# Performance work log

Measured on AMD Instinct MI355X. Metric: run time of the kernel, lower is better.

## Reference

```python
import jax, jax.numpy as jnp
import numpy as np

N_HOPS = 3
N_NODES = 500000  # n_users + n_items


def setup_inputs() -> dict:
    key = jax.random.key(0)
    k1, k2, k3, k4, k5 = jax.random.split(key, 5)
    n_users, n_items, d, nnz = 100000, 400000, 64, 1250000
    return {
        "user_embed": jax.random.normal(k1, (n_users, d), dtype=jnp.float32),
        "item_embed": jax.random.normal(k2, (n_items, d), dtype=jnp.float32),
        "adj_row": jax.random.randint(k3, (nnz,), 0, n_users + n_items, dtype=jnp.int32),
        "adj_col": jax.random.randint(k4, (nnz,), 0, n_users + n_items, dtype=jnp.int32),
        "adj_val": jax.random.uniform(k5, (nnz,), dtype=jnp.float32),
        "n_users": n_users,
    }


def reference(user_embed, item_embed, adj_row, adj_col, adj_val, n_users):
    # all_embed: [N, d]
    all_embed = jnp.concatenate([user_embed, item_embed], axis=0)

    def spmm(x):
        # sparse @ dense: gather source-node features, scale by edge value,
        # scatter-add into destination rows. COO SpMM == SpecialSpmm.
        msgs = adj_val[:, None] * x[adj_col]          # [nnz, d]
        return jax.ops.segment_sum(msgs, adj_row, num_segments=N_NODES)

    agg = all_embed
    embs = [all_embed]
    for _ in range(N_HOPS):
        agg = spmm(agg)
        embs.append(agg)
    embs = jnp.stack(embs, axis=1)  # [N, n_hops+1, d]
    return embs[:n_users], embs[n_users:]
```

## Files before the change

### kernel.cpp

```cpp
#include <hip/hip_runtime.h>


#define DFEAT 64
#define ELLW 8

typedef float f32x4 __attribute__((ext_vector_type(4)));

__global__ void gc_zero(int4* __restrict__ p, int n4) {
    int i = blockIdx.x * blockDim.x + threadIdx.x;
    if (i < n4) p[i] = make_int4(0, 0, 0, 0);
}

__global__ void gc_fat(const float4* __restrict__ user4,
                       const float4* __restrict__ item4,
                       float4* __restrict__ out4,
                       const int* __restrict__ row, const int* __restrict__ col,
                       const float* __restrict__ val,
                       int* __restrict__ cnt, float2* __restrict__ ell,
                       int* __restrict__ ovfcnt, int4* __restrict__ ovf,
                       int n_users, int n_nodes, int nnz, int initB) {
    int b = blockIdx.x;
    if (b < initB) {
        int tid = b * blockDim.x + threadIdx.x;
        if (tid >= n_nodes * 16) return;
        int node = tid >> 4;
        int q = tid & 15;
        float4 v = (node < n_users) ? user4[(size_t)node * 16 + q]
                                    : item4[(size_t)(node - n_users) * 16 + q];
        out4[(size_t)node * 64 + q] = v;
    } else {
        int i = (b - initB) * blockDim.x + threadIdx.x;
        if (i >= nnz) return;
        int r = row[i];
        int pos = atomicAdd(&cnt[r], 1);
        int cq = col[i] << 6;
        if (pos < ELLW) {
            ell[(size_t)r * ELLW + pos] = make_float2(__int_as_float(cq), val[i]);
        } else {
            int o = atomicAdd(ovfcnt, 1);
            ovf[o] = make_int4(r, cq, __float_as_int(val[i]), 0);
        }
    }
}

__global__ void gc_hop(const int* __restrict__ cnt,
                       const float4* __restrict__ ell4,
                       float* __restrict__ out, int hop, int n_nodes) {
    int tid = blockIdx.x * blockDim.x + threadIdx.x;
    int l = tid & 7;
    int r = tid >> 3;
    if (r >= n_nodes) return;
    int c = cnt[r];
    if (c > ELLW) c = ELLW;
    const float4* src4 = (const float4*)out;
    int lane_off = (hop - 1) * 16 + l * 2;
    float4 a0 = make_float4(0.f, 0.f, 0.f, 0.f);
    float4 a1 = make_float4(0.f, 0.f, 0.f, 0.f);
    int e = 0;
    for (; e + 2 <= c; e += 2) {
        float4 s = ell4[(size_t)r * (ELLW / 2) + (e >> 1)];
        int i0 = __float_as_int(s.x) + lane_off;
        int i1 = __float_as_int(s.z) + lane_off;
        float4 x0a = src4[i0], x0b = src4[i0 + 1];
        float4 x1a = src4[i1], x1b = src4[i1 + 1];
        float v0 = s.y, v1 = s.w;
        a0.x += v0 * x0a.x; a0.y += v0 * x0a.y; a0.z += v0 * x0a.z; a0.w += v0 * x0a.w;
        a1.x += v0 * x0b.x; a1.y += v0 * x0b.y; a1.z += v0 * x0b.z; a1.w += v0 * x0b.w;
        a0.x += v1 * x1a.x; a0.y += v1 * x1a.y; a0.z += v1 * x1a.z; a0.w += v1 * x1a.w;
        a1.x += v1 * x1b.x; a1.y += v1 * x1b.y; a1.z += v1 * x1b.z; a1.w += v1 * x1b.w;
    }
    if (e < c) {
        float2 s = ((const float2*)ell4)[(size_t)r * ELLW + e];
        int i0 = __float_as_int(s.x) + lane_off;
        float4 x0a = src4[i0], x0b = src4[i0 + 1];
        float v0 = s.y;
        a0.x += v0 * x0a.x; a0.y += v0 * x0a.y; a0.z += v0 * x0a.z; a0.w += v0 * x0a.w;
        a1.x += v0 * x0b.x; a1.y += v0 * x0b.y; a1.z += v0 * x0b.z; a1.w += v0 * x0b.w;
    }
    size_t dq = (size_t)r * 64 + (size_t)hop * 16 + l * 2;
    float4* o4 = (float4*)out;
    if (hop == 3) {
        f32x4 n0 = {a0.x, a0.y, a0.z, a0.w};
        f32x4 n1 = {a1.x, a1.y, a1.z, a1.w};
        __builtin_nontemporal_store(n0, (f32x4*)o4 + dq);
        __builtin_nontemporal_store(n1, (f32x4*)o4 + dq + 1);
    } else {
        o4[dq] = a0;
        o4[dq + 1] = a1;
    }
}

__global__ void gc_ovf(const int* __restrict__ ovfcnt, const int4* __restrict__ ovf,
                       float* __restrict__ out, int hop) {
    int gtid = blockIdx.x * blockDim.x + threadIdx.x;
    int wave = gtid >> 6;
    int lane = gtid & 63;
    int nw = (gridDim.x * blockDim.x) >> 6;
    int cntv = *ovfcnt;
    size_t src_base = (size_t)(hop - 1) * 64 + lane;
    size_t dst_base = (size_t)hop * 64 + lane;
    for (int e = wave; e < cntv; e += nw) {
        int4 ed = ovf[e];
        int r = ed.x;
        int cq = ed.y;
        float v = __int_as_float(ed.z);
        float x = out[(size_t)cq * 4 + src_base];
        unsafeAtomicAdd(&out[(size_t)r * 256 + dst_base], v * x);
    }
}

__global__ void gc_init_out_full(const float4* __restrict__ user4,
                                 const float4* __restrict__ item4,
                                 float4* __restrict__ out4,
                                 int n_users, int n_nodes) {
    int tid = blockIdx.x * blockDim.x + threadIdx.x;
    if (tid >= n_nodes * 16) return;
    int node = tid >> 4;
    int q = tid & 15;
    float4 v = (node < n_users) ? user4[(size_t)node * 16 + q]
                                : item4[(size_t)(node - n_users) * 16 + q];
    float4 z = make_float4(0.f, 0.f, 0.f, 0.f);
    float4* p = out4 + (size_t)node * 64 + q;
    p[0] = v; p[16] = z; p[32] = z; p[48] = z;
}

__global__ void gc_spmm_atomic(const int* __restrict__ adj_row,
                               const int* __restrict__ adj_col,
                               const float* __restrict__ adj_val,
                               float* __restrict__ out, int hop, int nnz) {
    long long tid = (long long)blockIdx.x * blockDim.x + threadIdx.x;
    int e = (int)(tid >> 6);
    int j = (int)(tid & 63);
    if (e >= nnz) return;
    int r = adj_row[e];
    int c = adj_col[e];
    float v = adj_val[e];
    float x = out[(size_t)c * 256 + (size_t)(hop - 1) * 64 + j];
    unsafeAtomicAdd(&out[(size_t)r * 256 + (size_t)hop * 64 + j], v * x);
}

extern "C" void kernel_launch(void* const* d_in, const int* in_sizes, int n_in,
                              void* d_out, int out_size, void* d_ws, size_t ws_size,
                              hipStream_t stream) {
    const float* user_embed = (const float*)d_in[0];
    const float* item_embed = (const float*)d_in[1];
    const int*   adj_row    = (const int*)d_in[2];
    const int*   adj_col    = (const int*)d_in[3];
    const float* adj_val    = (const float*)d_in[4];
    const int n_users = in_sizes[0] / DFEAT;
    const int n_items = in_sizes[1] / DFEAT;
    const int n_nodes = n_users + n_items;
    const int nnz     = in_sizes[2];
    float* out = (float*)d_out;
    float4* out4 = (float4*)out;

    const int threads = 256;

    size_t off = 0;
    auto carve = [&](size_t bytes) { size_t o = off; off = (off + bytes + 255) & ~(size_t)255; return o; };
    size_t o_cnt    = carve((size_t)n_nodes * 4);
    size_t o_ovfcnt = carve(256);
    size_t zero_end = off;
    size_t o_ell    = carve((size_t)n_nodes * ELLW * 8);
    size_t o_ovf    = carve((size_t)nnz * 16);
    size_t needed = off;

    if (ws_size < needed) {
        int init_blocks = (n_nodes * 16 + threads - 1) / threads;
        hipLaunchKernelGGL(gc_init_out_full, dim3(init_blocks), dim3(threads), 0, stream,
                           (const float4*)user_embed, (const float4*)item_embed,
                           out4, n_users, n_nodes);
        long long spmm_total = (long long)nnz * 64;
        int spmm_blocks = (int)((spmm_total + threads - 1) / threads);
        for (int h = 1; h <= 3; ++h) {
            hipLaunchKernelGGL(gc_spmm_atomic, dim3(spmm_blocks), dim3(threads), 0, stream,
                               adj_row, adj_col, adj_val, out, h, nnz);
        }
        return;
    }

    char* ws = (char*)d_ws;
    int*    cnt    = (int*)(ws + o_cnt);
    int*    ovfcnt = (int*)(ws + o_ovfcnt);
    float2* ell    = (float2*)(ws + o_ell);
    int4*   ovf    = (int4*)(ws + o_ovf);

    int zn4 = (int)((zero_end - o_cnt) / 16);
    int zero_blocks = (zn4 + threads - 1) / threads;
    hipLaunchKernelGGL(gc_zero, dim3(zero_blocks), dim3(threads), 0, stream,
                       (int4*)(ws + o_cnt), zn4);

    int initB = (n_nodes * 16 + threads - 1) / threads;
    int scatB = (nnz + threads - 1) / threads;
    hipLaunchKernelGGL(gc_fat, dim3(initB + scatB), dim3(threads), 0, stream,
                       (const float4*)user_embed, (const float4*)item_embed, out4,
                       adj_row, adj_col, adj_val, cnt, ell, ovfcnt, ovf,
                       n_users, n_nodes, nnz, initB);

    long long hop_threads = (long long)n_nodes * 8;
    int hop_blocks = (int)((hop_threads + threads - 1) / threads);
    const int ovf_blocks = 256;
    for (int h = 1; h <= 3; ++h) {
        hipLaunchKernelGGL(gc_hop, dim3(hop_blocks), dim3(threads), 0, stream,
                           cnt, (const float4*)ell, out, h, n_nodes);
        hipLaunchKernelGGL(gc_ovf, dim3(ovf_blocks), dim3(threads), 0, stream,
                           ovfcnt, ovf, out, h);
    }
}
```

Before: 390.1 us.

## Gather neighbor features from bf16 shadow copies and widen ELL width

Keeps a bf16 shadow of each hop's embeddings (written alongside the fp32 output) and gathers neighbor rows from it in the SpMM hop, halving gathered bytes. ELL width grows from 8 to 12 so fewer edges fall into the atomic overflow path, and a fixup kernel refreshes shadow rows touched by overflow atomics. The fp32 output stores become nontemporal. This adds bf16 rounding error that compounds across hops, plus extra shadow writes and a small extra kernel per hop.

```diff
diff --git a/kernel.cpp b/kernel.cpp
--- a/kernel.cpp
+++ b/kernel.cpp
@@ -2,9 +2,20 @@
 
 
 #define DFEAT 64
-#define ELLW 8
+#define ELLW 12
 
 typedef float f32x4 __attribute__((ext_vector_type(4)));
+
+__device__ inline unsigned bf16rne(float x) {
+    unsigned u = __float_as_uint(x);
+    u += 0x7FFF + ((u >> 16) & 1);
+    return u;
+}
+__device__ inline unsigned pack2(float lo, float hi) {
+    return (bf16rne(lo) >> 16) | (bf16rne(hi) & 0xFFFF0000u);
+}
+__device__ inline float bflo(unsigned w) { return __uint_as_float(w << 16); }
+__device__ inline float bfhi(unsigned w) { return __uint_as_float(w & 0xFFFF0000u); }
 
 __global__ void gc_zero(int4* __restrict__ p, int n4) {
     int i = blockIdx.x * blockDim.x + threadIdx.x;
@@ -13,7 +24,7 @@
 
 __global__ void gc_fat(const float4* __restrict__ user4,
                        const float4* __restrict__ item4,
-                       float4* __restrict__ out4,
+                       float4* __restrict__ out4, uint2* __restrict__ shadow0,
                        const int* __restrict__ row, const int* __restrict__ col,
                        const float* __restrict__ val,
                        int* __restrict__ cnt, float2* __restrict__ ell,
@@ -27,24 +38,27 @@
         int q = tid & 15;
         float4 v = (node < n_users) ? user4[(size_t)node * 16 + q]
                                     : item4[(size_t)(node - n_users) * 16 + q];
-        out4[(size_t)node * 64 + q] = v;
+        f32x4 nv = {v.x, v.y, v.z, v.w};
+        __builtin_nontemporal_store(nv, (f32x4*)(out4 + (size_t)node * 64 + q));
+        shadow0[(size_t)node * 16 + q] = make_uint2(pack2(v.x, v.y), pack2(v.z, v.w));
     } else {
         int i = (b - initB) * blockDim.x + threadIdx.x;
         if (i >= nnz) return;
         int r = row[i];
         int pos = atomicAdd(&cnt[r], 1);
-        int cq = col[i] << 6;
         if (pos < ELLW) {
-            ell[(size_t)r * ELLW + pos] = make_float2(__int_as_float(cq), val[i]);
+            ell[(size_t)r * ELLW + pos] = make_float2(__int_as_float(col[i] << 3), val[i]);
         } else {
             int o = atomicAdd(ovfcnt, 1);
-            ovf[o] = make_int4(r, cq, __float_as_int(val[i]), 0);
+            ovf[o] = make_int4(r, col[i] << 6, __float_as_int(val[i]), 0);
         }
     }
 }
 
 __global__ void gc_hop(const int* __restrict__ cnt,
                        const float4* __restrict__ ell4,
+                       const int4* __restrict__ ssrc,
+                       int4* __restrict__ sdst,
                        float* __restrict__ out, int hop, int n_nodes) {
     int tid = blockIdx.x * blockDim.x + threadIdx.x;
     int l = tid & 7;
@@ -52,41 +66,43 @@
     if (r >= n_nodes) return;
     int c = cnt[r];
     if (c > ELLW) c = ELLW;
-    const float4* src4 = (const float4*)out;
-    int lane_off = (hop - 1) * 16 + l * 2;
     float4 a0 = make_float4(0.f, 0.f, 0.f, 0.f);
     float4 a1 = make_float4(0.f, 0.f, 0.f, 0.f);
     int e = 0;
     for (; e + 2 <= c; e += 2) {
         float4 s = ell4[(size_t)r * (ELLW / 2) + (e >> 1)];
-        int i0 = __float_as_int(s.x) + lane_off;
-        int i1 = __float_as_int(s.z) + lane_off;
-        float4 x0a = src4[i0], x0b = src4[i0 + 1];
-        float4 x1a = src4[i1], x1b = src4[i1 + 1];
+        int i0 = __float_as_int(s.x) + l;
+        int i1 = __float_as_int(s.z) + l;
+        int4 g0 = ssrc[i0];
+        int4 g1 = ssrc[i1];
         float v0 = s.y, v1 = s.w;
-        a0.x += v0 * x0a.x; a0.y += v0 * x0a.y; a0.z += v0 * x0a.z; a0.w += v0 * x0a.w;
-        a1.x += v0 * x0b.x; a1.y += v0 * x0b.y; a1.z += v0 * x0b.z; a1.w += v0 * x0b.w;
-        a0.x += v1 * x1a.x; a0.y += v1 * x1a.y; a0.z += v1 * x1a.z; a0.w += v1 * x1a.w;
-        a1.x += v1 * x1b.x; a1.y += v1 * x1b.y; a1.z += v1 * x1b.z; a1.w += v1 * x1b.w;
+        a0.x += v0 * bflo(g0.x); a0.y += v0 * bfhi(g0.x);
+        a0.z += v0 * bflo(g0.y); a0.w += v0 * bfhi(g0.y);
+        a1.x += v0 * bflo(g0.z); a1.y += v0 * bfhi(g0.z);
+        a1.z += v0 * bflo(g0.w); a1.w += v0 * bfhi(g0.w);
+        a0.x += v1 * bflo(g1.x); a0.y += v1 * bfhi(g1.x);
+        a0.z += v1 * bflo(g1.y); a0.w += v1 * bfhi(g1.y);
+        a1.x += v1 * bflo(g1.z); a1.y += v1 * bfhi(g1.z);
+        a1.z += v1 * bflo(g1.w); a1.w += v1 * bfhi(g1.w);
     }
     if (e < c) {
         float2 s = ((const float2*)ell4)[(size_t)r * ELLW + e];
-        int i0 = __float_as_int(s.x) + lane_off;
-        float4 x0a = src4[i0], x0b = src4[i0 + 1];
+        int i0 = __float_as_int(s.x) + l;
+        int4 g0 = ssrc[i0];
         float v0 = s.y;
-        a0.x += v0 * x0a.x; a0.y += v0 * x0a.y; a0.z += v0 * x0a.z; a0.w += v0 * x0a.w;
-        a1.x += v0 * x0b.x; a1.y += v0 * x0b.y; a1.z += v0 * x0b.z; a1.w += v0 * x0b.w;
+        a0.x += v0 * bflo(g0.x); a0.y += v0 * bfhi(g0.x);
+        a0.z += v0 * bflo(g0.y); a0.w += v0 * bfhi(g0.y);
+        a1.x += v0 * bflo(g0.z); a1.y += v0 * bfhi(g0.z);
+        a1.z += v0 * bflo(g0.w); a1.w += v0 * bfhi(g0.w);
     }
     size_t dq = (size_t)r * 64 + (size_t)hop * 16 + l * 2;
-    float4* o4 = (float4*)out;
-    if (hop == 3) {
-        f32x4 n0 = {a0.x, a0.y, a0.z, a0.w};
-        f32x4 n1 = {a1.x, a1.y, a1.z, a1.w};
-        __builtin_nontemporal_store(n0, (f32x4*)o4 + dq);
-        __builtin_nontemporal_store(n1, (f32x4*)o4 + dq + 1);
-    } else {
-        o4[dq] = a0;
-        o4[dq + 1] = a1;
+    f32x4 n0 = {a0.x, a0.y, a0.z, a0.w};
+    f32x4 n1 = {a1.x, a1.y, a1.z, a1.w};
+    __builtin_nontemporal_store(n0, (f32x4*)((float4*)out) + dq);
+    __builtin_nontemporal_store(n1, (f32x4*)((float4*)out) + dq + 1);
+    if (sdst) {
+        sdst[(size_t)r * 8 + l] = make_int4(pack2(a0.x, a0.y), pack2(a0.z, a0.w),
+                                            pack2(a1.x, a1.y), pack2(a1.z, a1.w));
     }
 }
 
@@ -101,11 +117,20 @@
     size_t dst_base = (size_t)hop * 64 + lane;
     for (int e = wave; e < cntv; e += nw) {
         int4 ed = ovf[e];
-        int r = ed.x;
-        int cq = ed.y;
         float v = __int_as_float(ed.z);
-        float x = out[(size_t)cq * 4 + src_base];
-        unsafeAtomicAdd(&out[(size_t)r * 256 + dst_base], v * x);
+        float x = out[(size_t)ed.y * 4 + src_base];
+        unsafeAtomicAdd(&out[(size_t)ed.x * 256 + dst_base], v * x);
+    }
+}
+
+__global__ void gc_sfix(const int* __restrict__ ovfcnt, const int4* __restrict__ ovf,
+                        const float* __restrict__ out, unsigned short* __restrict__ shadow,
+                        int hop) {
+    int cntv = *ovfcnt;
+    for (int i = blockIdx.x; i < cntv; i += gridDim.x) {
+        int r = ovf[i].x;
+        float x = out[(size_t)r * 256 + (size_t)hop * 64 + threadIdx.x];
+        shadow[(size_t)r * 64 + threadIdx.x] = (unsigned short)(bf16rne(x) >> 16);
     }
 }
 
@@ -163,6 +188,8 @@
     size_t zero_end = off;
     size_t o_ell    = carve((size_t)n_nodes * ELLW * 8);
     size_t o_ovf    = carve((size_t)nnz * 16);
+    size_t o_shA    = carve((size_t)n_nodes * DFEAT * 2);
+    size_t o_shB    = carve((size_t)n_nodes * DFEAT * 2);
     size_t needed = off;
 
     if (ws_size < needed) {
@@ -184,6 +211,8 @@
     int*    ovfcnt = (int*)(ws + o_ovfcnt);
     float2* ell    = (float2*)(ws + o_ell);
     int4*   ovf    = (int4*)(ws + o_ovf);
+    char*   shA    = ws + o_shA;
+    char*   shB    = ws + o_shB;
 
     int zn4 = (int)((zero_end - o_cnt) / 16);
     int zero_blocks = (zn4 + threads - 1) / threads;
@@ -193,17 +222,27 @@
     int initB = (n_nodes * 16 + threads - 1) / threads;
     int scatB = (nnz + threads - 1) / threads;
     hipLaunchKernelGGL(gc_fat, dim3(initB + scatB), dim3(threads), 0, stream,
-                       (const float4*)user_embed, (const float4*)item_embed, out4,
+                       (const float4*)user_embed, (const float4*)item_embed,
+                       out4, (uint2*)shA,
                        adj_row, adj_col, adj_val, cnt, ell, ovfcnt, ovf,
                        n_users, n_nodes, nnz, initB);
 
     long long hop_threads = (long long)n_nodes * 8;
     int hop_blocks = (int)((hop_threads + threads - 1) / threads);
     const int ovf_blocks = 256;
+    char* scur = shA;
+    char* snext = shB;
     for (int h = 1; h <= 3; ++h) {
+        int4* sdst = (h < 3) ? (int4*)snext : (int4*)nullptr;
         hipLaunchKernelGGL(gc_hop, dim3(hop_blocks), dim3(threads), 0, stream,
-                           cnt, (const float4*)ell, out, h, n_nodes);
+                           cnt, (const float4*)ell, (const int4*)scur, sdst,
+                           out, h, n_nodes);
         hipLaunchKernelGGL(gc_ovf, dim3(ovf_blocks), dim3(threads), 0, stream,
                            ovfcnt, ovf, out, h);
-    }
-}
+        if (h < 3) {
+            hipLaunchKernelGGL(gc_sfix, dim3(256), dim3(64), 0, stream,
+                               ovfcnt, ovf, out, (unsigned short*)snext, h);
+            char* t = scur; scur = snext; snext = t;
+        }
+    }
+}
```

Result: faster. 326.6 us (-16.3%).
